# Performance work log

Measured on AMD Instinct MI355X. Metric: run time of the kernel, lower is better.

Reference implementation:

```python
import jax, jax.numpy as jnp
import numpy as np

THRESHOLD = 0.5
CONNECT_EPS = 0.1


def setup_inputs() -> dict:
    key = jax.random.key(0)
    ks = jax.random.split(key, 8)
    B, N, F = 4, 512, 128
    H = jax.random.normal(ks[0], (B, N, F), dtype=jnp.float32)
    A = jax.random.uniform(ks[1], (B, N, N), dtype=jnp.float32)
    s2f, sf = 1.0 / np.sqrt(2 * F), 1.0 / np.sqrt(F)
    dW1 = jax.random.normal(ks[2], (2 * F, F), dtype=jnp.float32) * s2f
    db1 = jnp.zeros((F,), dtype=jnp.float32)
    dW2 = jax.random.normal(ks[3], (F, 1), dtype=jnp.float32) * sf
    db2 = jnp.zeros((1,), dtype=jnp.float32)
    rW1 = jax.random.normal(ks[4], (2 * F + 1, F), dtype=jnp.float32) * s2f
    rb1 = jnp.zeros((F,), dtype=jnp.float32)
    rW2 = jax.random.normal(ks[5], (F, F), dtype=jnp.float32) * sf
    rb2 = jnp.zeros((F,), dtype=jnp.float32)
    return {"H": H, "A": A, "dW1": dW1, "db1": db1, "dW2": dW2, "db2": db2,
            "rW1": rW1, "rb1": rb1, "rW2": rW2, "rb2": rb2}


def reference(H, A, dW1, db1, dW2, db2, rW1, rb1, rW2, rb2):
    B, N, F = H.shape
    # Detector on pairs [H_i ; H_j]: split the first linear so we never build [B,N,N,2F].
    Hi = jnp.einsum('bnf,fh->bnh', H, dW1[:F])           # [B,N,F]
    Hj = jnp.einsum('bnf,fh->bnh', H, dW1[F:])           # [B,N,F]
    h = jax.nn.elu(Hi[:, :, None, :] + Hj[:, None, :, :] + db1)  # [B,N,N,F]
    scores = jax.nn.sigmoid(jnp.einsum('bijh,ho->bijo', h, dW2)[..., 0] + db2[0])  # [B,N,N]
    connected = A > CONNECT_EPS
    contradictions = jnp.where(connected, scores, 0.0)
    max_contra = contradictions.max(axis=-1)             # [B,N]
    contra_mask = max_contra > THRESHOLD                 # [B,N] bool
    # Neighbor mean over A > 0 (strict zero, matching torch.where(A[b,n] > 0))
    nbr = (A > 0).astype(H.dtype)                        # [B,N,N]
    deg = nbr.sum(axis=-1)                               # [B,N]
    neighbor_feat = jnp.einsum('bij,bjf->bif', nbr, H) / jnp.maximum(deg, 1.0)[..., None]
    concat = jnp.concatenate([H, neighbor_feat, max_contra[..., None]], axis=-1)  # [B,N,2F+1]
    res = jax.nn.elu(jnp.einsum('bnf,fh->bnh', concat, rW1) + rb1)
    res = jnp.einsum('bnh,ho->bno', res, rW2) + rb2       # [B,N,F]
    update = contra_mask & (deg > 0)
    H_resolved = jnp.where(update[..., None], res, H)
    return H_resolved, contra_mask
```

## Files before the change

kernel.cpp:

```cpp
#include <hip/hip_runtime.h>
#include <cmath>

#define B_ 4
#define N_ 512
#define F_ 128
#define BN_ (B_*N_)
#define NG_ (BN_/4)

__device__ __forceinline__ float elu_f(float x) {
    return fmaxf(x, __expf(fminf(x, 0.f)) - 1.f);
}

__global__ __launch_bounds__(512, 4) void k_pre(
    const float* __restrict__ H, const float* __restrict__ dW1,
    const float* __restrict__ db1,
    float* __restrict__ Hi, float* __restrict__ EHi, float* __restrict__ HjT,
    float* __restrict__ csp) {
    __shared__ float sH[4][F_];
    __shared__ float sPA[3][4][F_], sPB[3][4][F_];
    const int t = threadIdx.x;
    const int f = t & 127;
    const int kq = t >> 7;
    if (blockIdx.x < NG_) {
        const int row0 = blockIdx.x * 4;
        const int b  = row0 >> 9;
        const int n0 = row0 & 511;
        sH[kq][f] = H[(size_t)(row0 + kq) * F_ + f];
        __syncthreads();
        float accA[4] = {0.f,0.f,0.f,0.f}, accB[4] = {0.f,0.f,0.f,0.f};
        const int k0 = kq * 32;
        #pragma unroll 4
        for (int k = k0; k < k0 + 32; ++k) {
            const float wa = dW1[(size_t)k * F_ + f];
            const float wb = dW1[(size_t)(F_ + k) * F_ + f];
            #pragma unroll
            for (int r = 0; r < 4; ++r) {
                accA[r] = fmaf(sH[r][k], wa, accA[r]);
                accB[r] = fmaf(sH[r][k], wb, accB[r]);
            }
        }
        if (kq > 0) {
            #pragma unroll
            for (int r = 0; r < 4; ++r) {
                sPA[kq - 1][r][f] = accA[r];
                sPB[kq - 1][r][f] = accB[r];
            }
        }
        __syncthreads();
        if (kq == 0) {
            const float bias = db1[f];
            float bsum[4];
            #pragma unroll
            for (int r = 0; r < 4; ++r) {
                const float av = accA[r] + sPA[0][r][f] + sPA[1][r][f]
                               + sPA[2][r][f] + bias;
                Hi [(size_t)(row0 + r) * F_ + f] = av;
                EHi[(size_t)(row0 + r) * F_ + f] = __expf(av);
                bsum[r] = accB[r] + sPB[0][r][f] + sPB[1][r][f] + sPB[2][r][f];
            }
            float4 hv;
            hv.x = bsum[0]; hv.y = bsum[1]; hv.z = bsum[2]; hv.w = bsum[3];
            *reinterpret_cast<float4*>(HjT + ((size_t)b * F_ + f) * N_ + n0) = hv;
        }
    } else {
        const int bx = blockIdx.x - NG_;
        const int b  = bx >> 3;
        const int e  = bx & 7;
        float s = 0.f;
        const float* hp = H + ((size_t)b * N_ + e * 64 + kq * 16) * F_ + f;
        #pragma unroll 4
        for (int jj = 0; jj < 16; ++jj) s += hp[(size_t)jj * F_];
        sH[kq][f] = s;
        __syncthreads();
        if (kq == 0)
            csp[((size_t)b * 8 + e) * F_ + f] =
                sH[0][f] + sH[1][f] + sH[2][f] + sH[3][f];
    }
}

__global__ __launch_bounds__(512, 4) void k_score(
    const float* __restrict__ Hi, const float* __restrict__ EHi,
    const float* __restrict__ HjT, const float* __restrict__ A,
    const float* __restrict__ dW2, const float* __restrict__ db2,
    float* __restrict__ maxcv, float* __restrict__ degv,
    unsigned long long* __restrict__ zmask, float* __restrict__ maskout) {
    __shared__ float4 sU[32][9];
    __shared__ float red_mx[8][4];
    __shared__ int   red_cnt[8][4];
    const int t = threadIdx.x;
    const int lane = t & 63;
    const int w = t >> 6;
    const int bi0 = blockIdx.x * 4;
    const int b = bi0 >> 9;

    if (t < 288) {
        const int q  = t / 9;
        const int sl = t - q * 9;
        const float* src = (sl < 4) ? (Hi  + (size_t)(bi0 + sl)     * F_ + 4 * q)
                         : (sl < 8) ? (EHi + (size_t)(bi0 + sl - 4) * F_ + 4 * q)
                                    : (dW2 + 4 * q);
        sU[q][sl] = *reinterpret_cast<const float4*>(src);
    }
    float a_r[4];
    #pragma unroll
    for (int r = 0; r < 4; ++r) a_r[r] = A[(size_t)(bi0 + r) * N_ + t];

    const float* __restrict__ hjp = HjT + (size_t)b * F_ * N_ + t;
    float hjA[4], hjB[4];
    #pragma unroll
    for (int s = 0; s < 4; ++s) hjA[s] = hjp[(size_t)s * N_];
    __syncthreads();

    float acc0 = 0.f, acc1 = 0.f, acc2 = 0.f, acc3 = 0.f;
    auto compQ = [&](int q, const float (&hjv)[4]) {
        const float4 h0 = sU[q][0], h1 = sU[q][1], h2 = sU[q][2], h3 = sU[q][3];
        const float4 e0 = sU[q][4], e1 = sU[q][5], e2 = sU[q][6], e3 = sU[q][7];
        const float4 wq = sU[q][8];
        const float* h0p = &h0.x; const float* h1p = &h1.x;
        const float* h2p = &h2.x; const float* h3p = &h3.x;
        const float* e0p = &e0.x; const float* e1p = &e1.x;
        const float* e2p = &e2.x; const float* e3p = &e3.x;
        const float* wqp = &wq.x;
        #pragma unroll
        for (int s = 0; s < 4; ++s) {
            const float hj = hjv[s];
            const float ej = __expf(hj);
            const float wv = wqp[s];
            acc0 = fmaf(__builtin_amdgcn_fmed3f(h0p[s] + hj,
                        fmaf(e0p[s], ej, -1.f), 0.f), wv, acc0);
            acc1 = fmaf(__builtin_amdgcn_fmed3f(h1p[s] + hj,
                        fmaf(e1p[s], ej, -1.f), 0.f), wv, acc1);
            acc2 = fmaf(__builtin_amdgcn_fmed3f(h2p[s] + hj,
                        fmaf(e2p[s], ej, -1.f), 0.f), wv, acc2);
            acc3 = fmaf(__builtin_amdgcn_fmed3f(h3p[s] + hj,
                        fmaf(e3p[s], ej, -1.f), 0.f), wv, acc3);
        }
    };
    auto loadhj = [&](int q, float (&buf)[4]) {
        #pragma unroll
        for (int s = 0; s < 4; ++s) buf[s] = hjp[(size_t)(4 * q + s) * N_];
    };
    for (int q = 0; q < 32; q += 2) {
        loadhj(q + 1, hjB);
        compQ(q, hjA);
        if (q + 2 < 32) loadhj(q + 2, hjA);
        compQ(q + 1, hjB);
    }

    float accv[4] = {acc0, acc1, acc2, acc3};
    #pragma unroll
    for (int r = 0; r < 4; ++r) {
        const float a = a_r[r];
        float mx = (a > 0.1f) ? accv[r] : -INFINITY;
        #pragma unroll
        for (int off = 1; off < 64; off <<= 1)
            mx = fmaxf(mx, __shfl_xor(mx, off));
        const unsigned long long pos = __ballot(a > 0.f);
        const unsigned long long zb  = __ballot(a <= 0.f);
        if (lane == 0) {
            red_mx[w][r]  = mx;
            red_cnt[w][r] = (int)__popcll(pos);
            zmask[(size_t)(bi0 + r) * 8 + w] = zb;
        }
    }
    __syncthreads();
    if (t < 4) {
        float m = -INFINITY; int c = 0;
        #pragma unroll
        for (int ww = 0; ww < 8; ++ww) {
            m = fmaxf(m, red_mx[ww][t]);
            c += red_cnt[ww][t];
        }
        const float mc = (m > -INFINITY)
                       ? 1.f / (1.f + __expf(-(m + db2[0]))) : 0.f;
        maxcv[bi0 + t] = mc;
        degv[bi0 + t]  = (float)c;
        maskout[bi0 + t] = (mc > 0.5f) ? 1.f : 0.f;
    }
}

__global__ __launch_bounds__(512, 4) void k_mlp(
    const float* __restrict__ H, const float* __restrict__ csp,
    const unsigned long long* __restrict__ zmask,
    const float* __restrict__ degv, const float* __restrict__ maxcv,
    const float* __restrict__ rW1, const float* __restrict__ rb1,
    const float* __restrict__ rW2, const float* __restrict__ rb2,
    float* __restrict__ out) {
    __shared__ float sC[4][260];
    __shared__ float sP[3][4][F_];
    __shared__ float sL1[4][F_];
    __shared__ float sMC[4], sDegF[4];
    const int t  = threadIdx.x;
    const int f  = t & 127;
    const int kq = t >> 7;
    const int row0 = blockIdx.x * 4;
    const int b = row0 >> 9;

    {
        const int row = row0 + kq;
        sC[kq][f] = H[(size_t)row * F_ + f];
        float cs = 0.f;
        #pragma unroll
        for (int e = 0; e < 8; ++e)
            cs += csp[((size_t)b * 8 + e) * F_ + f];
        #pragma unroll
        for (int wv = 0; wv < 8; ++wv) {
            unsigned long long zb = zmask[(size_t)row * 8 + wv];
            while (zb) {
                const int j = __ffsll(zb) - 1;
                zb &= zb - 1;
                cs -= H[((size_t)b * N_ + wv * 64 + j) * F_ + f];
            }
        }
        sC[kq][F_ + f] = cs / fmaxf(degv[row], 1.f);
    }
    if (t < 4) {
        sMC[t]   = maxcv[row0 + t];
        sDegF[t] = degv[row0 + t];
    }
    __syncthreads();

    float macc[4];
    {
        const float bias = rb1[f];
        #pragma unroll
        for (int r = 0; r < 4; ++r) macc[r] = (kq == 0) ? bias : 0.f;
    }
    const int k0 = kq * 64;
    #pragma unroll 4
    for (int k = k0; k < k0 + 64; ++k) {
        const float wv = rW1[(size_t)k * F_ + f];
        #pragma unroll
        for (int r = 0; r < 4; ++r) macc[r] = fmaf(sC[r][k], wv, macc[r]);
    }
    if (kq == 3) {
        const float w256 = rW1[(size_t)256 * F_ + f];
        #pragma unroll
        for (int r = 0; r < 4; ++r) macc[r] = fmaf(sMC[r], w256, macc[r]);
    }
    if (kq > 0) {
        #pragma unroll
        for (int r = 0; r < 4; ++r) sP[kq - 1][r][f] = macc[r];
    }
    __syncthreads();
    if (kq == 0) {
        #pragma unroll
        for (int r = 0; r < 4; ++r)
            sL1[r][f] = elu_f(macc[r] + sP[0][r][f] + sP[1][r][f] + sP[2][r][f]);
    }
    __syncthreads();

    float macc2[4];
    {
        const float bias2 = rb2[f];
        #pragma unroll
        for (int r = 0; r < 4; ++r) macc2[r] = (kq == 0) ? bias2 : 0.f;
    }
    const int m0k = kq * 32;
    #pragma unroll 4
    for (int k = m0k; k < m0k + 32; ++k) {
        const float wv = rW2[(size_t)k * F_ + f];
        #pragma unroll
        for (int r = 0; r < 4; ++r) macc2[r] = fmaf(sL1[r][k], wv, macc2[r]);
    }
    if (kq > 0) {
        #pragma unroll
        for (int r = 0; r < 4; ++r) sP[kq - 1][r][f] = macc2[r];
    }
    __syncthreads();
    if (kq == 0) {
        #pragma unroll
        for (int r = 0; r < 4; ++r) {
            const int row = row0 + r;
            const float res = macc2[r] + sP[0][r][f] + sP[1][r][f] + sP[2][r][f];
            const bool upd = (sMC[r] > 0.5f) && (sDegF[r] > 0.f);
            out[(size_t)row * F_ + f] = upd ? res : sC[r][f];
        }
    }
}

extern "C" void kernel_launch(void* const* d_in, const int* in_sizes, int n_in,
                              void* d_out, int out_size, void* d_ws, size_t ws_size,
                              hipStream_t stream) {
    const float* H   = (const float*)d_in[0];
    const float* A   = (const float*)d_in[1];
    const float* dW1 = (const float*)d_in[2];
    const float* db1 = (const float*)d_in[3];
    const float* dW2 = (const float*)d_in[4];
    const float* db2 = (const float*)d_in[5];
    const float* rW1 = (const float*)d_in[6];
    const float* rb1 = (const float*)d_in[7];
    const float* rW2 = (const float*)d_in[8];
    const float* rb2 = (const float*)d_in[9];

    float* ws   = (float*)d_ws;
    float* Hi   = ws;
    float* EHi  = Hi   + BN_ * F_;
    float* HjT  = EHi  + BN_ * F_;
    float* csp  = HjT  + BN_ * F_;
    float* degv = csp  + B_ * 8 * F_;
    float* maxc = degv + BN_;
    unsigned long long* zmask =
        (unsigned long long*)(maxc + BN_);

    float* out      = (float*)d_out;
    float* mask_out = out + BN_ * F_;

    k_pre  <<<NG_ + 32, 512, 0, stream>>>(H, dW1, db1, Hi, EHi, HjT, csp);
    k_score<<<NG_, 512, 0, stream>>>(Hi, EHi, HjT, A, dW2, db2,
                                     maxc, degv, zmask, mask_out);
    k_mlp  <<<NG_, 512, 0, stream>>>(H, csp, zmask, degv, maxc,
                                     rW1, rb1, rW2, rb2, out);
}
```

Baseline: 40.12 us.

## Split score reduction over feature quarters with float4 j-tiles and LDS combine

Rework k_score so each thread handles four adjacent j columns using float4 loads of HjT, with the 128 features split into four groups across thread quarters. Each thread therefore reads each sU shared-memory value once per four j instead of once per j. Partial sums go into a 32KB shared array and are combined after an extra barrier. This cuts LDS traffic and widens global loads, at the cost of more registers (16 accumulators plus float4 buffers), more shared memory (which may lower occupancy), and an extra synchronisation.

```diff
diff --git a/kernel.cpp b/kernel.cpp
--- a/kernel.cpp
+++ b/kernel.cpp
@@ -85,11 +85,14 @@
     float* __restrict__ maxcv, float* __restrict__ degv,
     unsigned long long* __restrict__ zmask, float* __restrict__ maskout) {
     __shared__ float4 sU[32][9];
-    __shared__ float red_mx[8][4];
-    __shared__ int   red_cnt[8][4];
+    __shared__ float  sAcc[4][4][N_];
+    __shared__ float  red_mx[8][4];
+    __shared__ int    red_cnt[8][4];
     const int t = threadIdx.x;
     const int lane = t & 63;
     const int w = t >> 6;
+    const int u  = t & 127;
+    const int kq = t >> 7;
     const int bi0 = blockIdx.x * 4;
     const int b = bi0 >> 9;
 
@@ -105,53 +108,74 @@
     #pragma unroll
     for (int r = 0; r < 4; ++r) a_r[r] = A[(size_t)(bi0 + r) * N_ + t];
 
-    const float* __restrict__ hjp = HjT + (size_t)b * F_ * N_ + t;
-    float hjA[4], hjB[4];
-    #pragma unroll
-    for (int s = 0; s < 4; ++s) hjA[s] = hjp[(size_t)s * N_];
-    __syncthreads();
-
-    float acc0 = 0.f, acc1 = 0.f, acc2 = 0.f, acc3 = 0.f;
-    auto compQ = [&](int q, const float (&hjv)[4]) {
+    const float* __restrict__ hjq = HjT + (size_t)b * F_ * N_
+                                  + (size_t)(kq * 32) * N_ + 4 * u;
+    float4 hjA[4], hjB[4];
+    #pragma unroll
+    for (int s = 0; s < 4; ++s)
+        hjA[s] = *reinterpret_cast<const float4*>(hjq + (size_t)s * N_);
+    __syncthreads();
+
+    float4 acc[4];
+    #pragma unroll
+    for (int r = 0; r < 4; ++r) acc[r] = make_float4(0.f, 0.f, 0.f, 0.f);
+
+    auto compF = [&](const float4& hj4, float hi0, float hi1, float hi2,
+                     float hi3, float ei0, float ei1, float ei2, float ei3,
+                     float wv) {
+        const float ejx = __expf(hj4.x), ejy = __expf(hj4.y),
+                    ejz = __expf(hj4.z), ejw = __expf(hj4.w);
+        const float* hip[4] = {&hi0, &hi1, &hi2, &hi3};
+        const float* eip[4] = {&ei0, &ei1, &ei2, &ei3};
+        #pragma unroll
+        for (int r = 0; r < 4; ++r) {
+            const float hi = *hip[r], ei = *eip[r];
+            acc[r].x = fmaf(__builtin_amdgcn_fmed3f(hi + hj4.x,
+                            fmaf(ei, ejx, -1.f), 0.f), wv, acc[r].x);
+            acc[r].y = fmaf(__builtin_amdgcn_fmed3f(hi + hj4.y,
+                            fmaf(ei, ejy, -1.f), 0.f), wv, acc[r].y);
+            acc[r].z = fmaf(__builtin_amdgcn_fmed3f(hi + hj4.z,
+                            fmaf(ei, ejz, -1.f), 0.f), wv, acc[r].z);
+            acc[r].w = fmaf(__builtin_amdgcn_fmed3f(hi + hj4.w,
+                            fmaf(ei, ejw, -1.f), 0.f), wv, acc[r].w);
+        }
+    };
+    auto compQ = [&](int qq, const float4 (&hjv)[4]) {
+        const int q = kq * 8 + qq;
         const float4 h0 = sU[q][0], h1 = sU[q][1], h2 = sU[q][2], h3 = sU[q][3];
         const float4 e0 = sU[q][4], e1 = sU[q][5], e2 = sU[q][6], e3 = sU[q][7];
         const float4 wq = sU[q][8];
-        const float* h0p = &h0.x; const float* h1p = &h1.x;
-        const float* h2p = &h2.x; const float* h3p = &h3.x;
-        const float* e0p = &e0.x; const float* e1p = &e1.x;
-        const float* e2p = &e2.x; const float* e3p = &e3.x;
-        const float* wqp = &wq.x;
-        #pragma unroll
-        for (int s = 0; s < 4; ++s) {
-            const float hj = hjv[s];
-            const float ej = __expf(hj);
-            const float wv = wqp[s];
-            acc0 = fmaf(__builtin_amdgcn_fmed3f(h0p[s] + hj,
-                        fmaf(e0p[s], ej, -1.f), 0.f), wv, acc0);
-            acc1 = fmaf(__builtin_amdgcn_fmed3f(h1p[s] + hj,
-                        fmaf(e1p[s], ej, -1.f), 0.f), wv, acc1);
-            acc2 = fmaf(__builtin_amdgcn_fmed3f(h2p[s] + hj,
-                        fmaf(e2p[s], ej, -1.f), 0.f), wv, acc2);
-            acc3 = fmaf(__builtin_amdgcn_fmed3f(h3p[s] + hj,
-                        fmaf(e3p[s], ej, -1.f), 0.f), wv, acc3);
-        }
+        compF(hjv[0], h0.x, h1.x, h2.x, h3.x, e0.x, e1.x, e2.x, e3.x, wq.x);
+        compF(hjv[1], h0.y, h1.y, h2.y, h3.y, e0.y, e1.y, e2.y, e3.y, wq.y);
+        compF(hjv[2], h0.z, h1.z, h2.z, h3.z, e0.z, e1.z, e2.z, e3.z, wq.z);
+        compF(hjv[3], h0.w, h1.w, h2.w, h3.w, e0.w, e1.w, e2.w, e3.w, wq.w);
     };
-    auto loadhj = [&](int q, float (&buf)[4]) {
-        #pragma unroll
-        for (int s = 0; s < 4; ++s) buf[s] = hjp[(size_t)(4 * q + s) * N_];
+    auto loadQ = [&](int qq, float4 (&buf)[4]) {
+        #pragma unroll
+        for (int s = 0; s < 4; ++s)
+            buf[s] = *reinterpret_cast<const float4*>(
+                hjq + (size_t)(qq * 4 + s) * N_);
     };
-    for (int q = 0; q < 32; q += 2) {
-        loadhj(q + 1, hjB);
-        compQ(q, hjA);
-        if (q + 2 < 32) loadhj(q + 2, hjA);
-        compQ(q + 1, hjB);
-    }
-
-    float accv[4] = {acc0, acc1, acc2, acc3};
+
+    #pragma unroll
+    for (int qq = 0; qq < 8; qq += 2) {
+        loadQ(qq + 1, hjB);
+        compQ(qq, hjA);
+        if (qq + 2 < 8) loadQ(qq + 2, hjA);
+        compQ(qq + 1, hjB);
+    }
+
+    #pragma unroll
+    for (int r = 0; r < 4; ++r)
+        *reinterpret_cast<float4*>(&sAcc[kq][r][4 * u]) = acc[r];
+    __syncthreads();
+
     #pragma unroll
     for (int r = 0; r < 4; ++r) {
         const float a = a_r[r];
-        float mx = (a > 0.1f) ? accv[r] : -INFINITY;
+        const float sum = sAcc[0][r][t] + sAcc[1][r][t]
+                        + sAcc[2][r][t] + sAcc[3][r][t];
+        float mx = (a > 0.1f) ? sum : -INFINITY;
         #pragma unroll
         for (int off = 1; off < 64; off <<= 1)
             mx = fmaxf(mx, __shfl_xor(mx, off));
```

New measurement: 152.3 us. 3.8x slower.
